# Optimization experiments

Hardware: AMD Instinct MI355X
Metric: run time of the kernel (lower is better)

Reference implementation:

```python
import jax, jax.numpy as jnp
import numpy as np

N_ENT = 100000
D = 128
N_EDGES = 1600000
B = 8192
EPS = 1e-5


def setup_inputs() -> dict:
    key = jax.random.key(0)
    ks = jax.random.split(key, 12)
    return {
        "E": jax.random.normal(ks[0], (N_ENT, D), jnp.float32),
        "gamma": jnp.ones((D,), jnp.float32),
        "beta": jnp.zeros((D,), jnp.float32),
        "W_gnn": jax.random.normal(ks[1], (D, D), jnp.float32) / np.sqrt(D),
        "b_gnn": jnp.zeros((D,), jnp.float32),
        "W_g": jax.random.normal(ks[2], (D,), jnp.float32) / np.sqrt(D),
        "b_g": jnp.zeros((), jnp.float32),
        "W_age": jax.random.normal(ks[3], (D, 7), jnp.float32) / np.sqrt(D),
        "b_age": jnp.zeros((7,), jnp.float32),
        "W_occ": jax.random.normal(ks[4], (D, 21), jnp.float32) / np.sqrt(D),
        "b_occ": jnp.zeros((21,), jnp.float32),
        "src": jax.random.randint(ks[5], (N_EDGES,), 0, N_ENT, jnp.int32),
        "dst": jax.random.randint(ks[6], (N_EDGES,), 0, N_ENT, jnp.int32),
        "neighbor": jax.random.randint(ks[7], (B,), 0, N_ENT, jnp.int32),
        "gender": jax.random.randint(ks[8], (B,), 0, 2, jnp.int32),
        "age": jax.random.randint(ks[9], (B,), 0, 7, jnp.int32),
        "occupation": jax.random.randint(ks[10], (B,), 0, 21, jnp.int32),
    }


def reference(E, gamma, beta, W_gnn, b_gnn, W_g, b_g, W_age, b_age, W_occ, b_occ,
              src, dst, neighbor, gender, age, occupation):
    n = E.shape[0]
    # encoder (embedding of all nodes) -> batchnorm over node axis
    mu = jnp.mean(E, axis=0)
    var = jnp.var(E, axis=0)
    h = (E - mu) * jax.lax.rsqrt(var + EPS) * gamma + beta  # [N, D]
    # gnn: mean neighbor aggregation over edge list, then linear + relu
    agg = jax.ops.segment_sum(h[src], dst, num_segments=n)  # [N, D]
    deg = jax.ops.segment_sum(jnp.ones_like(src, jnp.float32), dst, num_segments=n)
    agg = agg / jnp.maximum(deg, 1.0)[:, None]
    h = jax.nn.relu(agg @ W_gnn + b_gnn)  # [N, D]
    # gather walked-to nodes; gradient-reversal layer is identity in forward
    u = h[neighbor]  # [B, D]
    gender_pred = u @ W_g + b_g            # [B]
    age_pred = u @ W_age + b_age           # [B, 7]
    occ_pred = u @ W_occ + b_occ           # [B, 21]
    # mode == 'gender': BCEWithLogitsLoss (mean)
    z = gender.astype(jnp.float32)
    x = gender_pred
    loss_adv = jnp.mean(jnp.maximum(x, 0.0) - x * z + jnp.log1p(jnp.exp(-jnp.abs(x))))
    return (loss_adv, age_pred, gender_pred, occ_pred)
```

## Files before the change

kernel.cpp:

```cpp
#include <hip/hip_runtime.h>
#include <hip/hip_bf16.h>
#include <math.h>

#define N_ENT   100000
#define DIM     128
#define N_EDGES 1600000
#define BATCH   8192
#define EPS     1e-5f
#define CAP     64
#define NSTAT_BLK   512

#define WS_SCALE     256
#define WS_SHIFT     384
#define WS_COUNT     512
#define WS_BCOUNT    528
#define WS_SLOTOF    8720
#define WS_BUCKET    108720
#define WS_SLOTHEAD  633008
#define WS_PARTIAL   895152

__global__ __launch_bounds__(256) void stats_init_kernel(const float4* __restrict__ E4,
                                                         const int* __restrict__ neighbor,
                                                         int* __restrict__ slot_of,
                                                         int* __restrict__ bcount,
                                                         float* __restrict__ out_loss,
                                                         float* __restrict__ partial) {
    int t = threadIdx.x;
    if (blockIdx.x >= NSTAT_BLK) {
        int n = (blockIdx.x - NSTAT_BLK) * 256 + t;
        if (n < BATCH) {
            bcount[n] = 0;
            slot_of[neighbor[n]] = n;
        }
        if (n == 0) out_loss[0] = 0.f;
        return;
    }
    int sid = blockIdx.x;
    int cg = t & 31;
    int rs = t >> 5;
    const int STRIDE = NSTAT_BLK * 8;
    float sx = 0.f, sy = 0.f, sz = 0.f, sw = 0.f;
    float qx = 0.f, qy = 0.f, qz = 0.f, qw = 0.f;
    const float4 z4 = make_float4(0.f, 0.f, 0.f, 0.f);
    for (int r = sid * 8 + rs; r < N_ENT; r += 8 * STRIDE) {
        float4 v[8];
#pragma unroll
        for (int k = 0; k < 8; ++k) {
            int rr = r + k * STRIDE;
            v[k] = (rr < N_ENT) ? E4[(size_t)rr * 32 + cg] : z4;
        }
#pragma unroll
        for (int k = 0; k < 8; ++k) {
            sx += v[k].x; sy += v[k].y; sz += v[k].z; sw += v[k].w;
            qx += v[k].x * v[k].x; qy += v[k].y * v[k].y;
            qz += v[k].z * v[k].z; qw += v[k].w * v[k].w;
        }
    }
    __shared__ float sh[8 * 256];
    sh[0 * 256 + t] = sx; sh[1 * 256 + t] = sy;
    sh[2 * 256 + t] = sz; sh[3 * 256 + t] = sw;
    sh[4 * 256 + t] = qx; sh[5 * 256 + t] = qy;
    sh[6 * 256 + t] = qz; sh[7 * 256 + t] = qw;
    __syncthreads();
    for (int o = 128; o >= 32; o >>= 1) {
        if (t < o) {
#pragma unroll
            for (int j = 0; j < 8; ++j) sh[j * 256 + t] += sh[j * 256 + t + o];
        }
        __syncthreads();
    }
    if (t < 32) {
#pragma unroll
        for (int j = 0; j < 8; ++j)
            partial[sid * 256 + j * 32 + t] = sh[j * 256 + t];
    }
}

__global__ __launch_bounds__(256) void edge_finalize_kernel(const int4* __restrict__ src4,
                                                            const int4* __restrict__ dst4,
                                                            const int* __restrict__ slot_of,
                                                            int* __restrict__ bcount,
                                                            int* __restrict__ bucket,
                                                            const float* __restrict__ partial,
                                                            const float* __restrict__ gamma,
                                                            const float* __restrict__ beta,
                                                            float* __restrict__ scale,
                                                            float* __restrict__ shift) {
    if (blockIdx.x == 0) {
        int t = threadIdx.x;
        float s = 0.f;
#pragma unroll 16
        for (int b = 0; b < NSTAT_BLK; ++b) s += partial[b * 256 + t];
        __shared__ float tot[256];
        tot[t] = s;
        __syncthreads();
        if (t < 128) {
            int ti = t >> 2, j = t & 3;
            const float invn = 1.0f / (float)N_ENT;
            float mu = tot[j * 32 + ti] * invn;
            float var = tot[(j + 4) * 32 + ti] * invn - mu * mu;
            float rs = rsqrtf(var + EPS);
            float sc = gamma[t] * rs;
            scale[t] = sc;
            shift[t] = beta[t] - mu * sc;
        }
        return;
    }
    const int n4 = N_EDGES / 4;
    int tid = (blockIdx.x - 1) * blockDim.x + threadIdx.x;
    int e0 = tid * 2;
    int e1 = tid * 2 + 1;
    if (e0 >= n4) return;
    int4 d0 = dst4[e0];
    int4 s0 = src4[e0];
    bool has1 = (e1 < n4);
    int4 d1 = has1 ? dst4[e1] : make_int4(0, 0, 0, 0);
    int4 s1 = has1 ? src4[e1] : make_int4(0, 0, 0, 0);
    int sl0 = slot_of[d0.x];
    int sl1 = slot_of[d0.y];
    int sl2 = slot_of[d0.z];
    int sl3 = slot_of[d0.w];
    int sl4 = has1 ? slot_of[d1.x] : -1;
    int sl5 = has1 ? slot_of[d1.y] : -1;
    int sl6 = has1 ? slot_of[d1.z] : -1;
    int sl7 = has1 ? slot_of[d1.w] : -1;
    if (sl0 >= 0) { int p = atomicAdd(&bcount[sl0], 1); if (p < CAP) bucket[sl0 * CAP + p] = s0.x; }
    if (sl1 >= 0) { int p = atomicAdd(&bcount[sl1], 1); if (p < CAP) bucket[sl1 * CAP + p] = s0.y; }
    if (sl2 >= 0) { int p = atomicAdd(&bcount[sl2], 1); if (p < CAP) bucket[sl2 * CAP + p] = s0.z; }
    if (sl3 >= 0) { int p = atomicAdd(&bcount[sl3], 1); if (p < CAP) bucket[sl3 * CAP + p] = s0.w; }
    if (sl4 >= 0) { int p = atomicAdd(&bcount[sl4], 1); if (p < CAP) bucket[sl4 * CAP + p] = s1.x; }
    if (sl5 >= 0) { int p = atomicAdd(&bcount[sl5], 1); if (p < CAP) bucket[sl5 * CAP + p] = s1.y; }
    if (sl6 >= 0) { int p = atomicAdd(&bcount[sl6], 1); if (p < CAP) bucket[sl6 * CAP + p] = s1.z; }
    if (sl7 >= 0) { int p = atomicAdd(&bcount[sl7], 1); if (p < CAP) bucket[sl7 * CAP + p] = s1.w; }
}

#define HW_LD 132

__global__ __launch_bounds__(256) void gather_gemm_heads_kernel(const float4* __restrict__ E4,
                                                                const int* __restrict__ bcount,
                                                                const int* __restrict__ bucket,
                                                                const float* __restrict__ scale,
                                                                const float* __restrict__ shift,
                                                                const float4* __restrict__ W4,
                                                                const float4* __restrict__ bias4,
                                                                const float* __restrict__ W_g,
                                                                const float* __restrict__ b_g,
                                                                const float* __restrict__ W_age,
                                                                const float* __restrict__ b_age,
                                                                const float* __restrict__ W_occ,
                                                                const float* __restrict__ b_occ,
                                                                float* __restrict__ slot_heads) {
    __shared__ float A_s[32 * 128];
    __shared__ float HW[29 * HW_LD];
    __shared__ float hb[32];
    int t = threadIdx.x;
    int rowbase = blockIdx.x * 32;

    for (int idx = t; idx < 29 * 128; idx += 256) {
        int h = idx >> 7;
        int d = idx & 127;
        float v;
        if (h < 7)       v = W_age[d * 7 + h];
        else if (h < 28) v = W_occ[d * 21 + (h - 7)];
        else             v = W_g[d];
        HW[h * HW_LD + d] = v;
    }
    if (t < 29) hb[t] = (t < 7) ? b_age[t] : (t < 28) ? b_occ[t - 7] : b_g[0];

    {
        int wid = t >> 6;
        int lane = t & 63;
        int q = lane & 31;
        int sub = lane >> 5;
        for (int j = 0; j < 8; ++j) {
            int sl = wid * 8 + j;
            int slot = rowbase + sl;
            int dg = bcount[slot];
            int m = dg < CAP ? dg : CAP;
            const int* bk = bucket + slot * CAP;
            float ax = 0.f, ay = 0.f, az = 0.f, aw = 0.f;
            int i = sub;
            for (; i + 14 < m; i += 16) {
                int r0 = bk[i], r1 = bk[i + 2], r2 = bk[i + 4], r3 = bk[i + 6];
                int r4 = bk[i + 8], r5 = bk[i + 10], r6 = bk[i + 12], r7 = bk[i + 14];
                float4 v0 = E4[(size_t)r0 * 32 + q];
                float4 v1 = E4[(size_t)r1 * 32 + q];
                float4 v2 = E4[(size_t)r2 * 32 + q];
                float4 v3 = E4[(size_t)r3 * 32 + q];
                float4 v4 = E4[(size_t)r4 * 32 + q];
                float4 v5 = E4[(size_t)r5 * 32 + q];
                float4 v6 = E4[(size_t)r6 * 32 + q];
                float4 v7 = E4[(size_t)r7 * 32 + q];
                ax += v0.x + v1.x + v2.x + v3.x + v4.x + v5.x + v6.x + v7.x;
                ay += v0.y + v1.y + v2.y + v3.y + v4.y + v5.y + v6.y + v7.y;
                az += v0.z + v1.z + v2.z + v3.z + v4.z + v5.z + v6.z + v7.z;
                aw += v0.w + v1.w + v2.w + v3.w + v4.w + v5.w + v6.w + v7.w;
            }
            for (; i + 6 < m; i += 8) {
                int r0 = bk[i], r1 = bk[i + 2], r2 = bk[i + 4], r3 = bk[i + 6];
                float4 v0 = E4[(size_t)r0 * 32 + q];
                float4 v1 = E4[(size_t)r1 * 32 + q];
                float4 v2 = E4[(size_t)r2 * 32 + q];
                float4 v3 = E4[(size_t)r3 * 32 + q];
                ax += v0.x + v1.x + v2.x + v3.x;
                ay += v0.y + v1.y + v2.y + v3.y;
                az += v0.z + v1.z + v2.z + v3.z;
                aw += v0.w + v1.w + v2.w + v3.w;
            }
            for (; i < m; i += 2) {
                int r0 = bk[i];
                float4 v0 = E4[(size_t)r0 * 32 + q];
                ax += v0.x; ay += v0.y; az += v0.z; aw += v0.w;
            }
            ax += __shfl_down(ax, 32);
            ay += __shfl_down(ay, 32);
            az += __shfl_down(az, 32);
            aw += __shfl_down(aw, 32);
            if (sub == 0) {
                float4 o; o.x = ax; o.y = ay; o.z = az; o.w = aw;
                ((float4*)A_s)[sl * 32 + q] = o;
            }
        }
    }
    __syncthreads();

    const float4* sc4 = (const float4*)scale;
    const float4* sf4 = (const float4*)shift;
#pragma unroll
    for (int i = 0; i < 4; ++i) {
        int f4 = t + i * 256;
        int row = f4 >> 5;
        int cgl = f4 & 31;
        float fdg = (float)bcount[rowbase + row];
        float rd = 1.0f / fmaxf(fdg, 1.0f);
        float4 v = ((float4*)A_s)[f4];
        float4 sc = sc4[cgl];
        float4 sf = sf4[cgl];
        float4 o;
        o.x = (v.x * sc.x + fdg * sf.x) * rd;
        o.y = (v.y * sc.y + fdg * sf.y) * rd;
        o.z = (v.z * sc.z + fdg * sf.z) * rd;
        o.w = (v.w * sc.w + fdg * sf.w) * rd;
        ((float4*)A_s)[f4] = o;
    }
    __syncthreads();

    int cg = t & 31;
    int rg = t >> 5;
    int r0 = rg * 4;
    float acc[4][4] = {{0.f}};
#pragma unroll 4
    for (int k = 0; k < 128; ++k) {
        float4 wv = W4[k * 32 + cg];
#pragma unroll
        for (int i = 0; i < 4; ++i) {
            float a = A_s[(r0 + i) * 128 + k];
            acc[i][0] += a * wv.x;
            acc[i][1] += a * wv.y;
            acc[i][2] += a * wv.z;
            acc[i][3] += a * wv.w;
        }
    }
    float4 bv = bias4[cg];
    __syncthreads();
#pragma unroll
    for (int i = 0; i < 4; ++i) {
        float4 o;
        o.x = fmaxf(acc[i][0] + bv.x, 0.f);
        o.y = fmaxf(acc[i][1] + bv.y, 0.f);
        o.z = fmaxf(acc[i][2] + bv.z, 0.f);
        o.w = fmaxf(acc[i][3] + bv.w, 0.f);
        ((float4*)A_s)[(r0 + i) * 32 + cg] = o;
    }
    __syncthreads();

#pragma unroll
    for (int i = 0; i < 4; ++i) {
        int task = t + i * 256;
        int row = task >> 5;
        int h = task & 31;
        if (h < 29) {
            const float4* h4 = (const float4*)(A_s + row * 128);
            const float4* w4 = (const float4*)(HW + h * HW_LD);
            float a0 = hb[h], a1 = 0.f, a2 = 0.f, a3 = 0.f;
#pragma unroll 8
            for (int dd = 0; dd < 32; ++dd) {
                float4 hv = h4[dd];
                float4 wv = w4[dd];
                a0 += hv.x * wv.x;
                a1 += hv.y * wv.y;
                a2 += hv.z * wv.z;
                a3 += hv.w * wv.w;
            }
            slot_heads[(size_t)(rowbase + row) * 32 + h] = a0 + a1 + a2 + a3;
        }
    }
}

__global__ __launch_bounds__(256) void map_loss_kernel(const float* __restrict__ slot_heads,
                                                       const int* __restrict__ slot_of,
                                                       const int* __restrict__ neighbor,
                                                       const int* __restrict__ gender,
                                                       float* __restrict__ out_age,
                                                       float* __restrict__ out_gender,
                                                       float* __restrict__ out_occ,
                                                       float* __restrict__ out_loss) {
    int b = blockIdx.x * 256 + threadIdx.x;
    float val = 0.f;
    if (b < BATCH) {
        int slot = slot_of[neighbor[b]];
        const float* hs = slot_heads + (size_t)slot * 32;
#pragma unroll
        for (int c = 0; c < 7; ++c)  out_age[b * 7 + c] = hs[c];
#pragma unroll
        for (int c = 0; c < 21; ++c) out_occ[b * 21 + c] = hs[7 + c];
        float x = hs[28];
        out_gender[b] = x;
        float z = (float)gender[b];
        val = fmaxf(x, 0.f) - x * z + log1pf(expf(-fabsf(x)));
    }
    __shared__ float sh[256];
    sh[threadIdx.x] = val;
    __syncthreads();
    for (int o = 128; o > 0; o >>= 1) {
        if (threadIdx.x < o) sh[threadIdx.x] += sh[threadIdx.x + o];
        __syncthreads();
    }
    if (threadIdx.x == 0) atomicAdd(out_loss, sh[0] * (1.0f / (float)BATCH));
}

extern "C" void kernel_launch(void* const* d_in, const int* in_sizes, int n_in,
                              void* d_out, int out_size, void* d_ws, size_t ws_size,
                              hipStream_t stream) {
    const float* E      = (const float*)d_in[0];
    const float* gamma  = (const float*)d_in[1];
    const float* beta   = (const float*)d_in[2];
    const float* W_gnn  = (const float*)d_in[3];
    const float* b_gnn  = (const float*)d_in[4];
    const float* W_g    = (const float*)d_in[5];
    const float* b_g    = (const float*)d_in[6];
    const float* W_age  = (const float*)d_in[7];
    const float* b_age  = (const float*)d_in[8];
    const float* W_occ  = (const float*)d_in[9];
    const float* b_occ  = (const float*)d_in[10];
    const int*   src    = (const int*)d_in[11];
    const int*   dst    = (const int*)d_in[12];
    const int*   neigh  = (const int*)d_in[13];
    const int*   gender = (const int*)d_in[14];

    float* ws      = (float*)d_ws;
    int*   wsi     = (int*)d_ws;
    float* scale   = ws + WS_SCALE;
    float* shift   = ws + WS_SHIFT;
    int*   bcount  = wsi + WS_BCOUNT;
    int*   slot_of = wsi + WS_SLOTOF;
    int*   bucket  = wsi + WS_BUCKET;
    float* slot_hd = ws + WS_SLOTHEAD;
    float* partial = ws + WS_PARTIAL;

    float* out       = (float*)d_out;
    float* out_loss  = out;
    float* out_age   = out + 1;
    float* out_gen   = out + 1 + BATCH * 7;
    float* out_occ   = out + 1 + BATCH * 7 + BATCH;

    stats_init_kernel<<<NSTAT_BLK + BATCH / 256, 256, 0, stream>>>(
        (const float4*)E, neigh, slot_of, bcount, out_loss, partial);
    {
        const int n4 = N_EDGES / 4;
        int nthreads = (n4 + 1) / 2;
        int eblocks = (nthreads + 255) / 256;
        edge_finalize_kernel<<<1 + eblocks, 256, 0, stream>>>(
            (const int4*)src, (const int4*)dst, slot_of, bcount, bucket,
            partial, gamma, beta, scale, shift);
    }
    gather_gemm_heads_kernel<<<BATCH / 32, 256, 0, stream>>>(
        (const float4*)E, bcount, bucket, scale, shift,
        (const float4*)W_gnn, (const float4*)b_gnn,
        W_g, b_g, W_age, b_age, W_occ, b_occ, slot_hd);
    map_loss_kernel<<<BATCH / 256, 256, 0, stream>>>(slot_hd, slot_of, neigh, gender,
                                                     out_age, out_gen, out_occ, out_loss);
}
```

Before: 187.2 us.

## Fuse all stages into one persistent kernel with grid-wide atomic barriers

Merges the stats, edge bucketing, gather+GEMM+heads and loss stages into a single 1024-block kernel that separates phases with software grid barriers on an atomic counter. The BN partial reduction becomes two-level (16 blocks, then block 0), and the GEMM stage is re-tiled to 8 rows per block. This removes three kernel launch gaps in exchange for barrier spin overhead. It assumes all 1024 blocks are co-resident, which the launch bounds of 4 blocks per CU are meant to allow; otherwise it deadlocks.

```diff
diff --git a/kernel.cpp b/kernel.cpp
--- a/kernel.cpp
+++ b/kernel.cpp
@@ -1,5 +1,4 @@
 #include <hip/hip_runtime.h>
-#include <hip/hip_bf16.h>
 #include <math.h>
 
 #define N_ENT   100000
@@ -8,155 +7,160 @@
 #define BATCH   8192
 #define EPS     1e-5f
 #define CAP     64
-#define NSTAT_BLK   512
-
-#define WS_SCALE     256
-#define WS_SHIFT     384
-#define WS_COUNT     512
-#define WS_BCOUNT    528
-#define WS_SLOTOF    8720
-#define WS_BUCKET    108720
-#define WS_SLOTHEAD  633008
-#define WS_PARTIAL   895152
-
-__global__ __launch_bounds__(256) void stats_init_kernel(const float4* __restrict__ E4,
-                                                         const int* __restrict__ neighbor,
-                                                         int* __restrict__ slot_of,
-                                                         int* __restrict__ bcount,
-                                                         float* __restrict__ out_loss,
-                                                         float* __restrict__ partial) {
-    int t = threadIdx.x;
-    if (blockIdx.x >= NSTAT_BLK) {
-        int n = (blockIdx.x - NSTAT_BLK) * 256 + t;
-        if (n < BATCH) {
+#define NBLK    1024
+#define NTHR    256
+#define HW_LD   132
+
+#define WS_BAR      0
+#define WS_SCALE    16
+#define WS_SHIFT    144
+#define WS_P2       272
+#define WS_BCOUNT   4368
+#define WS_SLOTOF   12560
+#define WS_BUCKET   112560
+#define WS_SLOTHEAD 636848
+#define WS_PARTIAL  898992
+
+__device__ __forceinline__ void gsync(int* bar, int target) {
+    __syncthreads();
+    if (threadIdx.x == 0) {
+        __hip_atomic_fetch_add(bar, 1, __ATOMIC_ACQ_REL, __HIP_MEMORY_SCOPE_AGENT);
+        while (__hip_atomic_load(bar, __ATOMIC_ACQUIRE, __HIP_MEMORY_SCOPE_AGENT) < target) {
+            __builtin_amdgcn_s_sleep(8);
+        }
+    }
+    __syncthreads();
+}
+
+__global__ void init_bar_kernel(int* __restrict__ bar, float* __restrict__ out_loss) {
+    if (threadIdx.x == 0) {
+        __hip_atomic_store(bar, 0, __ATOMIC_RELAXED, __HIP_MEMORY_SCOPE_AGENT);
+        out_loss[0] = 0.f;
+    }
+}
+
+__global__ __launch_bounds__(NTHR, 4) void mega_kernel(
+    const float4* __restrict__ E4,
+    const int*    __restrict__ neighbor,
+    const int*    __restrict__ gender,
+    const int4*   __restrict__ src4,
+    const int4*   __restrict__ dst4,
+    const float*  __restrict__ gamma,
+    const float*  __restrict__ beta,
+    const float4* __restrict__ W4,
+    const float4* __restrict__ bias4,
+    const float*  __restrict__ W_g,
+    const float*  __restrict__ b_g,
+    const float*  __restrict__ W_age,
+    const float*  __restrict__ b_age,
+    const float*  __restrict__ W_occ,
+    const float*  __restrict__ b_occ,
+    int*   __restrict__ bar,
+    int*   __restrict__ slot_of,
+    int*   __restrict__ bcount,
+    int*   __restrict__ bucket,
+    float* __restrict__ scale,
+    float* __restrict__ shift,
+    float* __restrict__ partial,
+    float* __restrict__ p2,
+    float* __restrict__ slot_heads,
+    float* __restrict__ out_age,
+    float* __restrict__ out_gender,
+    float* __restrict__ out_occ,
+    float* __restrict__ out_loss)
+{
+    __shared__ __align__(16) float sh[8 * NTHR];
+    __shared__ __align__(16) float A_s[8 * 128];
+    __shared__ __align__(16) float HW[29 * HW_LD];
+    __shared__ float hb[32];
+    const int t = threadIdx.x;
+    const int bid = blockIdx.x;
+
+    {
+        const int cgc = t & 31;
+        const int rs  = t >> 5;
+        const int S = NBLK * 8;
+        float sx = 0.f, sy = 0.f, sz = 0.f, sw = 0.f;
+        float qx = 0.f, qy = 0.f, qz = 0.f, qw = 0.f;
+        const float4 z4 = make_float4(0.f, 0.f, 0.f, 0.f);
+        for (int r = bid * 8 + rs; r < N_ENT; r += 4 * S) {
+            int r1 = r + S, r2 = r + 2 * S, r3 = r + 3 * S;
+            float4 v0 = E4[(size_t)r * 32 + cgc];
+            float4 v1 = (r1 < N_ENT) ? E4[(size_t)r1 * 32 + cgc] : z4;
+            float4 v2 = (r2 < N_ENT) ? E4[(size_t)r2 * 32 + cgc] : z4;
+            float4 v3 = (r3 < N_ENT) ? E4[(size_t)r3 * 32 + cgc] : z4;
+            sx += v0.x + v1.x + v2.x + v3.x;
+            sy += v0.y + v1.y + v2.y + v3.y;
+            sz += v0.z + v1.z + v2.z + v3.z;
+            sw += v0.w + v1.w + v2.w + v3.w;
+            qx += v0.x * v0.x + v1.x * v1.x + v2.x * v2.x + v3.x * v3.x;
+            qy += v0.y * v0.y + v1.y * v1.y + v2.y * v2.y + v3.y * v3.y;
+            qz += v0.z * v0.z + v1.z * v1.z + v2.z * v2.z + v3.z * v3.z;
+            qw += v0.w * v0.w + v1.w * v1.w + v2.w * v2.w + v3.w * v3.w;
+        }
+        sh[0 * NTHR + t] = sx; sh[1 * NTHR + t] = sy;
+        sh[2 * NTHR + t] = sz; sh[3 * NTHR + t] = sw;
+        sh[4 * NTHR + t] = qx; sh[5 * NTHR + t] = qy;
+        sh[6 * NTHR + t] = qz; sh[7 * NTHR + t] = qw;
+        __syncthreads();
+        for (int o = 128; o >= 32; o >>= 1) {
+            if (t < o) {
+#pragma unroll
+                for (int j = 0; j < 8; ++j) sh[j * NTHR + t] += sh[j * NTHR + t + o];
+            }
+            __syncthreads();
+        }
+        if (t < 32) {
+#pragma unroll
+            for (int j = 0; j < 8; ++j)
+                partial[(size_t)bid * NTHR + j * 32 + t] = sh[j * NTHR + t];
+        }
+        if (bid >= NBLK - 32) {
+            int n = (bid - (NBLK - 32)) * NTHR + t;
             bcount[n] = 0;
             slot_of[neighbor[n]] = n;
         }
-        if (n == 0) out_loss[0] = 0.f;
-        return;
-    }
-    int sid = blockIdx.x;
-    int cg = t & 31;
-    int rs = t >> 5;
-    const int STRIDE = NSTAT_BLK * 8;
-    float sx = 0.f, sy = 0.f, sz = 0.f, sw = 0.f;
-    float qx = 0.f, qy = 0.f, qz = 0.f, qw = 0.f;
-    const float4 z4 = make_float4(0.f, 0.f, 0.f, 0.f);
-    for (int r = sid * 8 + rs; r < N_ENT; r += 8 * STRIDE) {
-        float4 v[8];
-#pragma unroll
-        for (int k = 0; k < 8; ++k) {
-            int rr = r + k * STRIDE;
-            v[k] = (rr < N_ENT) ? E4[(size_t)rr * 32 + cg] : z4;
-        }
-#pragma unroll
-        for (int k = 0; k < 8; ++k) {
-            sx += v[k].x; sy += v[k].y; sz += v[k].z; sw += v[k].w;
-            qx += v[k].x * v[k].x; qy += v[k].y * v[k].y;
-            qz += v[k].z * v[k].z; qw += v[k].w * v[k].w;
-        }
-    }
-    __shared__ float sh[8 * 256];
-    sh[0 * 256 + t] = sx; sh[1 * 256 + t] = sy;
-    sh[2 * 256 + t] = sz; sh[3 * 256 + t] = sw;
-    sh[4 * 256 + t] = qx; sh[5 * 256 + t] = qy;
-    sh[6 * 256 + t] = qz; sh[7 * 256 + t] = qw;
-    __syncthreads();
-    for (int o = 128; o >= 32; o >>= 1) {
-        if (t < o) {
-#pragma unroll
-            for (int j = 0; j < 8; ++j) sh[j * 256 + t] += sh[j * 256 + t + o];
-        }
-        __syncthreads();
-    }
-    if (t < 32) {
-#pragma unroll
-        for (int j = 0; j < 8; ++j)
-            partial[sid * 256 + j * 32 + t] = sh[j * 256 + t];
-    }
-}
-
-__global__ __launch_bounds__(256) void edge_finalize_kernel(const int4* __restrict__ src4,
-                                                            const int4* __restrict__ dst4,
-                                                            const int* __restrict__ slot_of,
-                                                            int* __restrict__ bcount,
-                                                            int* __restrict__ bucket,
-                                                            const float* __restrict__ partial,
-                                                            const float* __restrict__ gamma,
-                                                            const float* __restrict__ beta,
-                                                            float* __restrict__ scale,
-                                                            float* __restrict__ shift) {
-    if (blockIdx.x == 0) {
-        int t = threadIdx.x;
+    }
+    gsync(bar, 1 * NBLK);
+
+    if (bid < 16) {
+        const float* pp = partial + (size_t)bid * 64 * NTHR + t;
         float s = 0.f;
-#pragma unroll 16
-        for (int b = 0; b < NSTAT_BLK; ++b) s += partial[b * 256 + t];
-        __shared__ float tot[256];
-        tot[t] = s;
-        __syncthreads();
-        if (t < 128) {
-            int ti = t >> 2, j = t & 3;
-            const float invn = 1.0f / (float)N_ENT;
-            float mu = tot[j * 32 + ti] * invn;
-            float var = tot[(j + 4) * 32 + ti] * invn - mu * mu;
-            float rs = rsqrtf(var + EPS);
-            float sc = gamma[t] * rs;
-            scale[t] = sc;
-            shift[t] = beta[t] - mu * sc;
-        }
-        return;
-    }
-    const int n4 = N_EDGES / 4;
-    int tid = (blockIdx.x - 1) * blockDim.x + threadIdx.x;
-    int e0 = tid * 2;
-    int e1 = tid * 2 + 1;
-    if (e0 >= n4) return;
-    int4 d0 = dst4[e0];
-    int4 s0 = src4[e0];
-    bool has1 = (e1 < n4);
-    int4 d1 = has1 ? dst4[e1] : make_int4(0, 0, 0, 0);
-    int4 s1 = has1 ? src4[e1] : make_int4(0, 0, 0, 0);
-    int sl0 = slot_of[d0.x];
-    int sl1 = slot_of[d0.y];
-    int sl2 = slot_of[d0.z];
-    int sl3 = slot_of[d0.w];
-    int sl4 = has1 ? slot_of[d1.x] : -1;
-    int sl5 = has1 ? slot_of[d1.y] : -1;
-    int sl6 = has1 ? slot_of[d1.z] : -1;
-    int sl7 = has1 ? slot_of[d1.w] : -1;
-    if (sl0 >= 0) { int p = atomicAdd(&bcount[sl0], 1); if (p < CAP) bucket[sl0 * CAP + p] = s0.x; }
-    if (sl1 >= 0) { int p = atomicAdd(&bcount[sl1], 1); if (p < CAP) bucket[sl1 * CAP + p] = s0.y; }
-    if (sl2 >= 0) { int p = atomicAdd(&bcount[sl2], 1); if (p < CAP) bucket[sl2 * CAP + p] = s0.z; }
-    if (sl3 >= 0) { int p = atomicAdd(&bcount[sl3], 1); if (p < CAP) bucket[sl3 * CAP + p] = s0.w; }
-    if (sl4 >= 0) { int p = atomicAdd(&bcount[sl4], 1); if (p < CAP) bucket[sl4 * CAP + p] = s1.x; }
-    if (sl5 >= 0) { int p = atomicAdd(&bcount[sl5], 1); if (p < CAP) bucket[sl5 * CAP + p] = s1.y; }
-    if (sl6 >= 0) { int p = atomicAdd(&bcount[sl6], 1); if (p < CAP) bucket[sl6 * CAP + p] = s1.z; }
-    if (sl7 >= 0) { int p = atomicAdd(&bcount[sl7], 1); if (p < CAP) bucket[sl7 * CAP + p] = s1.w; }
-}
-
-#define HW_LD 132
-
-__global__ __launch_bounds__(256) void gather_gemm_heads_kernel(const float4* __restrict__ E4,
-                                                                const int* __restrict__ bcount,
-                                                                const int* __restrict__ bucket,
-                                                                const float* __restrict__ scale,
-                                                                const float* __restrict__ shift,
-                                                                const float4* __restrict__ W4,
-                                                                const float4* __restrict__ bias4,
-                                                                const float* __restrict__ W_g,
-                                                                const float* __restrict__ b_g,
-                                                                const float* __restrict__ W_age,
-                                                                const float* __restrict__ b_age,
-                                                                const float* __restrict__ W_occ,
-                                                                const float* __restrict__ b_occ,
-                                                                float* __restrict__ slot_heads) {
-    __shared__ float A_s[32 * 128];
-    __shared__ float HW[29 * HW_LD];
-    __shared__ float hb[32];
-    int t = threadIdx.x;
-    int rowbase = blockIdx.x * 32;
-
-    for (int idx = t; idx < 29 * 128; idx += 256) {
+#pragma unroll 8
+        for (int k = 0; k < 64; ++k) s += pp[(size_t)k * NTHR];
+        p2[bid * NTHR + t] = s;
+    } else {
+        const int n4c = N_EDGES / 4;
+        int tid = (bid - 16) * NTHR + t;
+        int e0 = tid * 2;
+        if (e0 < n4c) {
+            int e1 = e0 + 1;
+            int4 d0 = dst4[e0];
+            int4 s0 = src4[e0];
+            bool has1 = (e1 < n4c);
+            int4 d1 = has1 ? dst4[e1] : make_int4(0, 0, 0, 0);
+            int4 s1 = has1 ? src4[e1] : make_int4(0, 0, 0, 0);
+            int sl0 = slot_of[d0.x];
+            int sl1 = slot_of[d0.y];
+            int sl2 = slot_of[d0.z];
+            int sl3 = slot_of[d0.w];
+            int sl4 = has1 ? slot_of[d1.x] : -1;
+            int sl5 = has1 ? slot_of[d1.y] : -1;
+            int sl6 = has1 ? slot_of[d1.z] : -1;
+            int sl7 = has1 ? slot_of[d1.w] : -1;
+            if (sl0 >= 0) { int p = atomicAdd(&bcount[sl0], 1); if (p < CAP) bucket[sl0 * CAP + p] = s0.x; }
+            if (sl1 >= 0) { int p = atomicAdd(&bcount[sl1], 1); if (p < CAP) bucket[sl1 * CAP + p] = s0.y; }
+            if (sl2 >= 0) { int p = atomicAdd(&bcount[sl2], 1); if (p < CAP) bucket[sl2 * CAP + p] = s0.z; }
+            if (sl3 >= 0) { int p = atomicAdd(&bcount[sl3], 1); if (p < CAP) bucket[sl3 * CAP + p] = s0.w; }
+            if (sl4 >= 0) { int p = atomicAdd(&bcount[sl4], 1); if (p < CAP) bucket[sl4 * CAP + p] = s1.x; }
+            if (sl5 >= 0) { int p = atomicAdd(&bcount[sl5], 1); if (p < CAP) bucket[sl5 * CAP + p] = s1.y; }
+            if (sl6 >= 0) { int p = atomicAdd(&bcount[sl6], 1); if (p < CAP) bucket[sl6 * CAP + p] = s1.z; }
+            if (sl7 >= 0) { int p = atomicAdd(&bcount[sl7], 1); if (p < CAP) bucket[sl7 * CAP + p] = s1.w; }
+        }
+    }
+    gsync(bar, 2 * NBLK);
+
+    for (int idx = t; idx < 29 * 128; idx += NTHR) {
         int h = idx >> 7;
         int d = idx & 127;
         float v;
@@ -166,15 +170,31 @@
         HW[h * HW_LD + d] = v;
     }
     if (t < 29) hb[t] = (t < 7) ? b_age[t] : (t < 28) ? b_occ[t - 7] : b_g[0];
-
+    if (bid == 0) {
+        float s = 0.f;
+#pragma unroll
+        for (int k = 0; k < 16; ++k) s += p2[k * NTHR + t];
+        sh[t] = s;
+        __syncthreads();
+        if (t < 128) {
+            int ti = t >> 2, j = t & 3;
+            const float invn = 1.0f / (float)N_ENT;
+            float mu = sh[j * 32 + ti] * invn;
+            float var = sh[(j + 4) * 32 + ti] * invn - mu * mu;
+            float rsq = rsqrtf(var + EPS);
+            float sc = gamma[t] * rsq;
+            scale[t] = sc;
+            shift[t] = beta[t] - mu * sc;
+        }
+    }
     {
         int wid = t >> 6;
         int lane = t & 63;
         int q = lane & 31;
         int sub = lane >> 5;
-        for (int j = 0; j < 8; ++j) {
-            int sl = wid * 8 + j;
-            int slot = rowbase + sl;
+        for (int j = 0; j < 2; ++j) {
+            int sl = wid * 2 + j;
+            int slot = bid * 8 + sl;
             int dg = bcount[slot];
             int m = dg < CAP ? dg : CAP;
             const int* bk = bucket + slot * CAP;
@@ -222,111 +242,82 @@
             }
         }
     }
-    __syncthreads();
-
-    const float4* sc4 = (const float4*)scale;
-    const float4* sf4 = (const float4*)shift;
-#pragma unroll
-    for (int i = 0; i < 4; ++i) {
-        int f4 = t + i * 256;
-        int row = f4 >> 5;
-        int cgl = f4 & 31;
-        float fdg = (float)bcount[rowbase + row];
+    gsync(bar, 3 * NBLK);
+
+    {
+        const int row = t >> 5;
+        const int c4  = t & 31;
+        int slot = bid * 8 + row;
+        float fdg = (float)bcount[slot];
         float rd = 1.0f / fmaxf(fdg, 1.0f);
-        float4 v = ((float4*)A_s)[f4];
-        float4 sc = sc4[cgl];
-        float4 sf = sf4[cgl];
+        float4 v = ((float4*)A_s)[row * 32 + c4];
+        float4 sc = ((const float4*)scale)[c4];
+        float4 sf = ((const float4*)shift)[c4];
         float4 o;
         o.x = (v.x * sc.x + fdg * sf.x) * rd;
         o.y = (v.y * sc.y + fdg * sf.y) * rd;
         o.z = (v.z * sc.z + fdg * sf.z) * rd;
         o.w = (v.w * sc.w + fdg * sf.w) * rd;
-        ((float4*)A_s)[f4] = o;
-    }
-    __syncthreads();
-
-    int cg = t & 31;
-    int rg = t >> 5;
-    int r0 = rg * 4;
-    float acc[4][4] = {{0.f}};
+        ((float4*)A_s)[row * 32 + c4] = o;
+        __syncthreads();
+        float a0 = 0.f, a1 = 0.f, a2 = 0.f, a3 = 0.f;
 #pragma unroll 4
-    for (int k = 0; k < 128; ++k) {
-        float4 wv = W4[k * 32 + cg];
-#pragma unroll
-        for (int i = 0; i < 4; ++i) {
-            float a = A_s[(r0 + i) * 128 + k];
-            acc[i][0] += a * wv.x;
-            acc[i][1] += a * wv.y;
-            acc[i][2] += a * wv.z;
-            acc[i][3] += a * wv.w;
-        }
-    }
-    float4 bv = bias4[cg];
-    __syncthreads();
-#pragma unroll
-    for (int i = 0; i < 4; ++i) {
-        float4 o;
-        o.x = fmaxf(acc[i][0] + bv.x, 0.f);
-        o.y = fmaxf(acc[i][1] + bv.y, 0.f);
-        o.z = fmaxf(acc[i][2] + bv.z, 0.f);
-        o.w = fmaxf(acc[i][3] + bv.w, 0.f);
-        ((float4*)A_s)[(r0 + i) * 32 + cg] = o;
-    }
-    __syncthreads();
-
-#pragma unroll
-    for (int i = 0; i < 4; ++i) {
-        int task = t + i * 256;
-        int row = task >> 5;
-        int h = task & 31;
-        if (h < 29) {
+        for (int k = 0; k < 128; ++k) {
+            float a = A_s[row * 128 + k];
+            float4 wv = W4[k * 32 + c4];
+            a0 += a * wv.x; a1 += a * wv.y; a2 += a * wv.z; a3 += a * wv.w;
+        }
+        float4 bv = bias4[c4];
+        __syncthreads();
+        float4 o2;
+        o2.x = fmaxf(a0 + bv.x, 0.f);
+        o2.y = fmaxf(a1 + bv.y, 0.f);
+        o2.z = fmaxf(a2 + bv.z, 0.f);
+        o2.w = fmaxf(a3 + bv.w, 0.f);
+        ((float4*)A_s)[row * 32 + c4] = o2;
+        __syncthreads();
+        if (c4 < 29) {
             const float4* h4 = (const float4*)(A_s + row * 128);
-            const float4* w4 = (const float4*)(HW + h * HW_LD);
-            float a0 = hb[h], a1 = 0.f, a2 = 0.f, a3 = 0.f;
+            const float4* w4 = (const float4*)(HW + c4 * HW_LD);
+            float b0 = hb[c4], b1 = 0.f, b2 = 0.f, b3 = 0.f;
 #pragma unroll 8
             for (int dd = 0; dd < 32; ++dd) {
                 float4 hv = h4[dd];
                 float4 wv = w4[dd];
-                a0 += hv.x * wv.x;
-                a1 += hv.y * wv.y;
-                a2 += hv.z * wv.z;
-                a3 += hv.w * wv.w;
-            }
-            slot_heads[(size_t)(rowbase + row) * 32 + h] = a0 + a1 + a2 + a3;
-        }
-    }
-}
-
-__global__ __launch_bounds__(256) void map_loss_kernel(const float* __restrict__ slot_heads,
-                                                       const int* __restrict__ slot_of,
-                                                       const int* __restrict__ neighbor,
-                                                       const int* __restrict__ gender,
-                                                       float* __restrict__ out_age,
-                                                       float* __restrict__ out_gender,
-                                                       float* __restrict__ out_occ,
-                                                       float* __restrict__ out_loss) {
-    int b = blockIdx.x * 256 + threadIdx.x;
-    float val = 0.f;
-    if (b < BATCH) {
-        int slot = slot_of[neighbor[b]];
+                b0 += hv.x * wv.x;
+                b1 += hv.y * wv.y;
+                b2 += hv.z * wv.z;
+                b3 += hv.w * wv.w;
+            }
+            slot_heads[(size_t)slot * 32 + c4] = b0 + b1 + b2 + b3;
+        }
+    }
+    gsync(bar, 4 * NBLK);
+
+    {
+        int bi = bid * 8 + (t >> 5);
+        int c  = t & 31;
+        int slot = slot_of[neighbor[bi]];
         const float* hs = slot_heads + (size_t)slot * 32;
-#pragma unroll
-        for (int c = 0; c < 7; ++c)  out_age[b * 7 + c] = hs[c];
-#pragma unroll
-        for (int c = 0; c < 21; ++c) out_occ[b * 21 + c] = hs[7 + c];
-        float x = hs[28];
-        out_gender[b] = x;
-        float z = (float)gender[b];
-        val = fmaxf(x, 0.f) - x * z + log1pf(expf(-fabsf(x)));
-    }
-    __shared__ float sh[256];
-    sh[threadIdx.x] = val;
-    __syncthreads();
-    for (int o = 128; o > 0; o >>= 1) {
-        if (threadIdx.x < o) sh[threadIdx.x] += sh[threadIdx.x + o];
-        __syncthreads();
-    }
-    if (threadIdx.x == 0) atomicAdd(out_loss, sh[0] * (1.0f / (float)BATCH));
+        float val = 0.f;
+        if (c < 29) {
+            float x = hs[c];
+            if (c < 7)       out_age[bi * 7 + c] = x;
+            else if (c < 28) out_occ[bi * 21 + (c - 7)] = x;
+            else {
+                out_gender[bi] = x;
+                float z = (float)gender[bi];
+                val = fmaxf(x, 0.f) - x * z + log1pf(expf(-fabsf(x)));
+            }
+        }
+        sh[t] = val;
+        __syncthreads();
+        for (int o = 128; o > 0; o >>= 1) {
+            if (t < o) sh[t] += sh[t + o];
+            __syncthreads();
+        }
+        if (t == 0) atomicAdd(out_loss, sh[0] * (1.0f / (float)BATCH));
+    }
 }
 
 extern "C" void kernel_launch(void* const* d_in, const int* in_sizes, int n_in,
@@ -348,15 +339,17 @@
     const int*   neigh  = (const int*)d_in[13];
     const int*   gender = (const int*)d_in[14];
 
-    float* ws      = (float*)d_ws;
-    int*   wsi     = (int*)d_ws;
-    float* scale   = ws + WS_SCALE;
-    float* shift   = ws + WS_SHIFT;
-    int*   bcount  = wsi + WS_BCOUNT;
-    int*   slot_of = wsi + WS_SLOTOF;
-    int*   bucket  = wsi + WS_BUCKET;
-    float* slot_hd = ws + WS_SLOTHEAD;
-    float* partial = ws + WS_PARTIAL;
+    float* ws  = (float*)d_ws;
+    int*   wsi = (int*)d_ws;
+    int*   bar      = wsi + WS_BAR;
+    float* scale    = ws + WS_SCALE;
+    float* shift    = ws + WS_SHIFT;
+    float* p2       = ws + WS_P2;
+    int*   bcount   = wsi + WS_BCOUNT;
+    int*   slot_of  = wsi + WS_SLOTOF;
+    int*   bucket   = wsi + WS_BUCKET;
+    float* slot_hd  = ws + WS_SLOTHEAD;
+    float* partial  = ws + WS_PARTIAL;
 
     float* out       = (float*)d_out;
     float* out_loss  = out;
@@ -364,20 +357,12 @@
     float* out_gen   = out + 1 + BATCH * 7;
     float* out_occ   = out + 1 + BATCH * 7 + BATCH;
 
-    stats_init_kernel<<<NSTAT_BLK + BATCH / 256, 256, 0, stream>>>(
-        (const float4*)E, neigh, slot_of, bcount, out_loss, partial);
-    {
-        const int n4 = N_EDGES / 4;
-        int nthreads = (n4 + 1) / 2;
-        int eblocks = (nthreads + 255) / 256;
-        edge_finalize_kernel<<<1 + eblocks, 256, 0, stream>>>(
-            (const int4*)src, (const int4*)dst, slot_of, bcount, bucket,
-            partial, gamma, beta, scale, shift);
-    }
-    gather_gemm_heads_kernel<<<BATCH / 32, 256, 0, stream>>>(
-        (const float4*)E, bcount, bucket, scale, shift,
-        (const float4*)W_gnn, (const float4*)b_gnn,
-        W_g, b_g, W_age, b_age, W_occ, b_occ, slot_hd);
-    map_loss_kernel<<<BATCH / 256, 256, 0, stream>>>(slot_hd, slot_of, neigh, gender,
-                                                     out_age, out_gen, out_occ, out_loss);
+    init_bar_kernel<<<1, 64, 0, stream>>>(bar, out_loss);
+    mega_kernel<<<NBLK, NTHR, 0, stream>>>(
+        (const float4*)E, neigh, gender, (const int4*)src, (const int4*)dst,
+        gamma, beta, (const float4*)W_gnn, (const float4*)b_gnn,
+        W_g, b_g, W_age, b_age, W_occ, b_occ,
+        bar, slot_of, bcount, bucket, scale, shift,
+        partial, p2, slot_hd,
+        out_age, out_gen, out_occ, out_loss);
 }
```

Measured after the change: 708.0 us. 3.78x slower.

## Fuse gather-GEMM-heads with loss mapping into a per-item kernel

Applied to the files above, without the earlier changes.

Merges the per-slot gather/GEMM/heads kernel and the map/loss kernel into one kernel that works directly on 8 batch items per block. It looks up each item's slot, gathers the neighbour sum, normalises, applies the GNN linear layer and the heads, then writes outputs and the loss partial directly. This removes one launch and the slot_heads intermediate round trip, and raises the block count for better CU coverage. In exchange, each block now reloads W_gnn and the head weights for only 8 rows, which multiplies weight traffic, and items that share a neighbour are recomputed.

```diff
diff --git a/kernel.cpp b/kernel.cpp
--- a/kernel.cpp
+++ b/kernel.cpp
@@ -1,5 +1,4 @@
 #include <hip/hip_runtime.h>
-#include <hip/hip_bf16.h>
 #include <math.h>
 
 #define N_ENT   100000
@@ -8,15 +7,14 @@
 #define BATCH   8192
 #define EPS     1e-5f
 #define CAP     64
-#define NSTAT_BLK   512
+#define NSTAT_BLK 512
+#define HW_LD   132
 
 #define WS_SCALE     256
 #define WS_SHIFT     384
-#define WS_COUNT     512
 #define WS_BCOUNT    528
 #define WS_SLOTOF    8720
 #define WS_BUCKET    108720
-#define WS_SLOTHEAD  633008
 #define WS_PARTIAL   895152
 
 __global__ __launch_bounds__(256) void stats_init_kernel(const float4* __restrict__ E4,
@@ -134,28 +132,35 @@
     if (sl7 >= 0) { int p = atomicAdd(&bcount[sl7], 1); if (p < CAP) bucket[sl7 * CAP + p] = s1.w; }
 }
 
-#define HW_LD 132
-
-__global__ __launch_bounds__(256) void gather_gemm_heads_kernel(const float4* __restrict__ E4,
-                                                                const int* __restrict__ bcount,
-                                                                const int* __restrict__ bucket,
-                                                                const float* __restrict__ scale,
-                                                                const float* __restrict__ shift,
-                                                                const float4* __restrict__ W4,
-                                                                const float4* __restrict__ bias4,
-                                                                const float* __restrict__ W_g,
-                                                                const float* __restrict__ b_g,
-                                                                const float* __restrict__ W_age,
-                                                                const float* __restrict__ b_age,
-                                                                const float* __restrict__ W_occ,
-                                                                const float* __restrict__ b_occ,
-                                                                float* __restrict__ slot_heads) {
-    __shared__ float A_s[32 * 128];
-    __shared__ float HW[29 * HW_LD];
+__global__ __launch_bounds__(256) void item_fused_kernel(const float4* __restrict__ E4,
+                                                         const int* __restrict__ neighbor,
+                                                         const int* __restrict__ gender,
+                                                         const int* __restrict__ slot_of,
+                                                         const int* __restrict__ bcount,
+                                                         const int* __restrict__ bucket,
+                                                         const float* __restrict__ scale,
+                                                         const float* __restrict__ shift,
+                                                         const float4* __restrict__ W4,
+                                                         const float4* __restrict__ bias4,
+                                                         const float* __restrict__ W_g,
+                                                         const float* __restrict__ b_g,
+                                                         const float* __restrict__ W_age,
+                                                         const float* __restrict__ b_age,
+                                                         const float* __restrict__ W_occ,
+                                                         const float* __restrict__ b_occ,
+                                                         float* __restrict__ out_age,
+                                                         float* __restrict__ out_gender,
+                                                         float* __restrict__ out_occ,
+                                                         float* __restrict__ out_loss) {
+    __shared__ __align__(16) float A_s[8 * 128];
+    __shared__ __align__(16) float HW[29 * HW_LD];
+    __shared__ float sh[256];
     __shared__ float hb[32];
-    int t = threadIdx.x;
-    int rowbase = blockIdx.x * 32;
-
+    __shared__ int   cslot_s[8];
+    const int t = threadIdx.x;
+    const int item0 = blockIdx.x * 8;
+
+    if (t < 8) cslot_s[t] = slot_of[neighbor[item0 + t]];
     for (int idx = t; idx < 29 * 128; idx += 256) {
         int h = idx >> 7;
         int d = idx & 127;
@@ -166,18 +171,19 @@
         HW[h * HW_LD + d] = v;
     }
     if (t < 29) hb[t] = (t < 7) ? b_age[t] : (t < 28) ? b_occ[t - 7] : b_g[0];
+    __syncthreads();
 
     {
         int wid = t >> 6;
         int lane = t & 63;
         int q = lane & 31;
         int sub = lane >> 5;
-        for (int j = 0; j < 8; ++j) {
-            int sl = wid * 8 + j;
-            int slot = rowbase + sl;
-            int dg = bcount[slot];
+        for (int j = 0; j < 2; ++j) {
+            int li = wid * 2 + j;
+            int cs = cslot_s[li];
+            int dg = bcount[cs];
             int m = dg < CAP ? dg : CAP;
-            const int* bk = bucket + slot * CAP;
+            const int* bk = bucket + cs * CAP;
             float ax = 0.f, ay = 0.f, az = 0.f, aw = 0.f;
             int i = sub;
             for (; i + 14 < m; i += 16) {
@@ -218,115 +224,80 @@
             aw += __shfl_down(aw, 32);
             if (sub == 0) {
                 float4 o; o.x = ax; o.y = ay; o.z = az; o.w = aw;
-                ((float4*)A_s)[sl * 32 + q] = o;
+                ((float4*)A_s)[li * 32 + q] = o;
             }
         }
     }
     __syncthreads();
 
-    const float4* sc4 = (const float4*)scale;
-    const float4* sf4 = (const float4*)shift;
-#pragma unroll
-    for (int i = 0; i < 4; ++i) {
-        int f4 = t + i * 256;
-        int row = f4 >> 5;
-        int cgl = f4 & 31;
-        float fdg = (float)bcount[rowbase + row];
+    const int row = t >> 5;
+    const int c4  = t & 31;
+    {
+        int cs = cslot_s[row];
+        float fdg = (float)bcount[cs];
         float rd = 1.0f / fmaxf(fdg, 1.0f);
-        float4 v = ((float4*)A_s)[f4];
-        float4 sc = sc4[cgl];
-        float4 sf = sf4[cgl];
+        float4 v = ((float4*)A_s)[row * 32 + c4];
+        float4 sc = ((const float4*)scale)[c4];
+        float4 sf = ((const float4*)shift)[c4];
         float4 o;
         o.x = (v.x * sc.x + fdg * sf.x) * rd;
         o.y = (v.y * sc.y + fdg * sf.y) * rd;
         o.z = (v.z * sc.z + fdg * sf.z) * rd;
         o.w = (v.w * sc.w + fdg * sf.w) * rd;
-        ((float4*)A_s)[f4] = o;
-    }
-    __syncthreads();
-
-    int cg = t & 31;
-    int rg = t >> 5;
-    int r0 = rg * 4;
-    float acc[4][4] = {{0.f}};
+        ((float4*)A_s)[row * 32 + c4] = o;
+    }
+    __syncthreads();
+
+    {
+        float a0 = 0.f, a1 = 0.f, a2 = 0.f, a3 = 0.f;
 #pragma unroll 4
-    for (int k = 0; k < 128; ++k) {
-        float4 wv = W4[k * 32 + cg];
-#pragma unroll
-        for (int i = 0; i < 4; ++i) {
-            float a = A_s[(r0 + i) * 128 + k];
-            acc[i][0] += a * wv.x;
-            acc[i][1] += a * wv.y;
-            acc[i][2] += a * wv.z;
-            acc[i][3] += a * wv.w;
-        }
-    }
-    float4 bv = bias4[cg];
-    __syncthreads();
-#pragma unroll
-    for (int i = 0; i < 4; ++i) {
-        float4 o;
-        o.x = fmaxf(acc[i][0] + bv.x, 0.f);
-        o.y = fmaxf(acc[i][1] + bv.y, 0.f);
-        o.z = fmaxf(acc[i][2] + bv.z, 0.f);
-        o.w = fmaxf(acc[i][3] + bv.w, 0.f);
-        ((float4*)A_s)[(r0 + i) * 32 + cg] = o;
-    }
-    __syncthreads();
-
-#pragma unroll
-    for (int i = 0; i < 4; ++i) {
-        int task = t + i * 256;
-        int row = task >> 5;
-        int h = task & 31;
-        if (h < 29) {
-            const float4* h4 = (const float4*)(A_s + row * 128);
-            const float4* w4 = (const float4*)(HW + h * HW_LD);
-            float a0 = hb[h], a1 = 0.f, a2 = 0.f, a3 = 0.f;
+        for (int k = 0; k < 128; ++k) {
+            float a = A_s[row * 128 + k];
+            float4 wv = W4[k * 32 + c4];
+            a0 += a * wv.x; a1 += a * wv.y; a2 += a * wv.z; a3 += a * wv.w;
+        }
+        float4 bv = bias4[c4];
+        __syncthreads();
+        float4 o2;
+        o2.x = fmaxf(a0 + bv.x, 0.f);
+        o2.y = fmaxf(a1 + bv.y, 0.f);
+        o2.z = fmaxf(a2 + bv.z, 0.f);
+        o2.w = fmaxf(a3 + bv.w, 0.f);
+        ((float4*)A_s)[row * 32 + c4] = o2;
+    }
+    __syncthreads();
+
+    float val = 0.f;
+    if (c4 < 29) {
+        const float4* h4 = (const float4*)(A_s + row * 128);
+        const float4* w4 = (const float4*)(HW + c4 * HW_LD);
+        float b0 = hb[c4], b1 = 0.f, b2 = 0.f, b3 = 0.f;
 #pragma unroll 8
-            for (int dd = 0; dd < 32; ++dd) {
-                float4 hv = h4[dd];
-                float4 wv = w4[dd];
-                a0 += hv.x * wv.x;
-                a1 += hv.y * wv.y;
-                a2 += hv.z * wv.z;
-                a3 += hv.w * wv.w;
-            }
-            slot_heads[(size_t)(rowbase + row) * 32 + h] = a0 + a1 + a2 + a3;
-        }
-    }
-}
-
-__global__ __launch_bounds__(256) void map_loss_kernel(const float* __restrict__ slot_heads,
-                                                       const int* __restrict__ slot_of,
-                                                       const int* __restrict__ neighbor,
-                                                       const int* __restrict__ gender,
-                                                       float* __restrict__ out_age,
-                                                       float* __restrict__ out_gender,
-                                                       float* __restrict__ out_occ,
-                                                       float* __restrict__ out_loss) {
-    int b = blockIdx.x * 256 + threadIdx.x;
-    float val = 0.f;
-    if (b < BATCH) {
-        int slot = slot_of[neighbor[b]];
-        const float* hs = slot_heads + (size_t)slot * 32;
-#pragma unroll
-        for (int c = 0; c < 7; ++c)  out_age[b * 7 + c] = hs[c];
-#pragma unroll
-        for (int c = 0; c < 21; ++c) out_occ[b * 21 + c] = hs[7 + c];
-        float x = hs[28];
-        out_gender[b] = x;
-        float z = (float)gender[b];
-        val = fmaxf(x, 0.f) - x * z + log1pf(expf(-fabsf(x)));
-    }
-    __shared__ float sh[256];
-    sh[threadIdx.x] = val;
+        for (int dd = 0; dd < 32; ++dd) {
+            float4 hv = h4[dd];
+            float4 wv = w4[dd];
+            b0 += hv.x * wv.x;
+            b1 += hv.y * wv.y;
+            b2 += hv.z * wv.z;
+            b3 += hv.w * wv.w;
+        }
+        float x = b0 + b1 + b2 + b3;
+        int item = item0 + row;
+        if (c4 < 7)       out_age[item * 7 + c4] = x;
+        else if (c4 < 28) out_occ[item * 21 + (c4 - 7)] = x;
+        else {
+            out_gender[item] = x;
+            float z = (float)gender[item];
+            val = fmaxf(x, 0.f) - x * z + log1pf(expf(-fabsf(x)));
+        }
+    }
+    sh[t] = val;
     __syncthreads();
     for (int o = 128; o > 0; o >>= 1) {
-        if (threadIdx.x < o) sh[threadIdx.x] += sh[threadIdx.x + o];
+        if (t < o) sh[t] += sh[t + o];
         __syncthreads();
     }
-    if (threadIdx.x == 0) atomicAdd(out_loss, sh[0] * (1.0f / (float)BATCH));
+    if (t == 0) atomicAdd(out_loss, sh[0] * (1.0f / (float)BATCH));
 }
 
 extern "C" void kernel_launch(void* const* d_in, const int* in_sizes, int n_in,
@@ -348,14 +319,13 @@
     const int*   neigh  = (const int*)d_in[13];
     const int*   gender = (const int*)d_in[14];
 
-    float* ws      = (float*)d_ws;
-    int*   wsi     = (int*)d_ws;
+    float* ws  = (float*)d_ws;
+    int*   wsi = (int*)d_ws;
     float* scale   = ws + WS_SCALE;
     float* shift   = ws + WS_SHIFT;
     int*   bcount  = wsi + WS_BCOUNT;
     int*   slot_of = wsi + WS_SLOTOF;
     int*   bucket  = wsi + WS_BUCKET;
-    float* slot_hd = ws + WS_SLOTHEAD;
     float* partial = ws + WS_PARTIAL;
 
     float* out       = (float*)d_out;
@@ -374,10 +344,9 @@
             (const int4*)src, (const int4*)dst, slot_of, bcount, bucket,
             partial, gamma, beta, scale, shift);
     }
-    gather_gemm_heads_kernel<<<BATCH / 32, 256, 0, stream>>>(
-        (const float4*)E, bcount, bucket, scale, shift,
+    item_fused_kernel<<<BATCH / 8, 256, 0, stream>>>(
+        (const float4*)E, neigh, gender, slot_of, bcount, bucket, scale, shift,
         (const float4*)W_gnn, (const float4*)b_gnn,
-        W_g, b_g, W_age, b_age, W_occ, b_occ, slot_hd);
-    map_loss_kernel<<<BATCH / 256, 256, 0, stream>>>(slot_hd, slot_of, neigh, gender,
-                                                     out_age, out_gen, out_occ, out_loss);
+        W_g, b_g, W_age, b_age, W_occ, b_occ,
+        out_age, out_gen, out_occ, out_loss);
 }
```

Result: no change. 189.8 us (+1.4%).
